# Kernel optimization log

Hardware: AMD Instinct MI355X
Metric: run time of the kernel (lower is better)

## Reference

```python
import jax, jax.numpy as jnp
import numpy as np

KD, KY, KX = 3, 3, 3  # kernel_size from init_kwargs


def setup_inputs() -> dict:
    key = jax.random.key(0)
    x = jax.random.normal(key, (4, 2, 64, 256, 256), dtype=jnp.float32)
    return {"x": x}


def reference(x):
    # x: [B, CH, D, H, W]
    B, CH, D, H, W = x.shape
    pd, py, px = (KD - 1) // 2, (KY - 1) // 2, (KX - 1) // 2
    # replicate padding (torch F.pad mode='replicate' == jnp.pad mode='edge')
    xp = jnp.pad(x, ((0, 0), (0, 0), (pd, pd), (py, py), (px, px)), mode='edge')
    center = (KD * KY * KX) // 2  # flattened center position, excluded from max
    # running max over the 26 non-center neighbors; never materializes the
    # [B, CH, 27, D, H, W] tensor the torch conv3d path creates.
    max_nc = jnp.full(x.shape, -jnp.inf, dtype=x.dtype)
    idx = 0
    for i in range(KD):
        for j in range(KY):
            for k in range(KX):
                if idx != center:
                    shifted = xp[:, :, i:i + D, j:j + H, k:k + W]
                    max_nc = jnp.maximum(max_nc, shifted)
                idx += 1
    mask = x > max_nc  # strict local maximum (excluding self)
    return x * mask.astype(x.dtype)
```

## Files before the change

kernel.cpp:

```cpp
#include <hip/hip_runtime.h>


constexpr int D_   = 64;
constexpr int H_   = 256;
constexpr int W_   = 256;
constexpr int HW_  = H_ * W_;
constexpr int NVOL = 8;
constexpr int DC   = 8;
constexpr int ROWS = 8;
constexpr int SROWS = ROWS + 2;

__device__ __forceinline__ float f3(float a, float b, float c) {
    return fmaxf(fmaxf(a, b), c);
}

__global__ __launch_bounds__(512, 4)
void nms3d(const float* __restrict__ x, float* __restrict__ out)
{
    __shared__ float buf[2][SROWS][W_];

    const int tx = threadIdx.x;
    const int ty = threadIdx.y;
    const int h0 = blockIdx.y * ROWS;
    const int h  = h0 + ty;
    const int n  = blockIdx.z;
    const int z0 = blockIdx.x * DC;
    const int c  = tx << 2;

    const float* __restrict__ base  = x   + (size_t)n * D_ * HW_;
    float* __restrict__       obase = out + (size_t)n * D_ * HW_;

    const int extra = (ty == 0) ? 0 : (ty == ROWS - 1 ? SROWS - 1 : -1);
    const int gx = (extra == 0) ? max(h0 - 1, 0) : min(h0 + ROWS, H_ - 1);

    {
        const float* sp = base + (size_t)max(z0 - 1, 0) * HW_;
        const float4 r = *(const float4*)(sp + h * W_ + c);
        *(float4*)&buf[0][ty + 1][c] = r;
        if (extra >= 0) {
            const float4 rx = *(const float4*)(sp + gx * W_ + c);
            *(float4*)&buf[0][extra][c] = rx;
        }
    }
    __syncthreads();

    float4 vm9_pp = {0,0,0,0};
    float4 vm9_p  = {0,0,0,0};
    float4 cr8_p  = {0,0,0,0};
    float4 vprev  = {0,0,0,0};

#pragma unroll
    for (int t = 0; t < DC + 2; ++t) {
        const int zi  = z0 - 1 + t;
        const int cur = t & 1, nxt = cur ^ 1;

        float4 r, rx;
        const bool do_stage = (t < DC + 1);
        if (do_stage) {
            const float* sp = base + (size_t)min(zi + 1, D_ - 1) * HW_;
            r = *(const float4*)(sp + h * W_ + c);
            if (extra >= 0) rx = *(const float4*)(sp + gx * W_ + c);
        }

        const float4 a = *(const float4*)&buf[cur][ty    ][c];
        const float4 b = *(const float4*)&buf[cur][ty + 1][c];
        const float4 d = *(const float4*)&buf[cur][ty + 2][c];

        float4 va;
        va.x = fmaxf(a.x, d.x); va.y = fmaxf(a.y, d.y);
        va.z = fmaxf(a.z, d.z); va.w = fmaxf(a.w, d.w);

        float vaL = __shfl_up(va.w, 1);   if (tx == 0)  vaL = va.x;
        float vaR = __shfl_down(va.x, 1); if (tx == 63) vaR = va.w;
        float bL  = __shfl_up(b.w, 1);    if (tx == 0)  bL  = b.x;
        float bR  = __shfl_down(b.x, 1);  if (tx == 63) bR  = b.w;

        float4 hv;
        hv.x = f3(vaL, va.x, va.y);  hv.y = f3(va.x, va.y, va.z);
        hv.z = f3(va.y, va.z, va.w); hv.w = f3(va.z, va.w, vaR);
        float4 nb;
        nb.x = fmaxf(bL, b.y);   nb.y = fmaxf(b.x, b.z);
        nb.z = fmaxf(b.y, b.w);  nb.w = fmaxf(b.z, bR);

        float4 c8, cu;
        c8.x = fmaxf(hv.x, nb.x); c8.y = fmaxf(hv.y, nb.y);
        c8.z = fmaxf(hv.z, nb.z); c8.w = fmaxf(hv.w, nb.w);
        cu.x = fmaxf(c8.x, b.x);  cu.y = fmaxf(c8.y, b.y);
        cu.z = fmaxf(c8.z, b.z);  cu.w = fmaxf(c8.w, b.w);

        if (zi > z0) {
            float4 mx, o;
            mx.x = f3(vm9_pp.x, cr8_p.x, cu.x);
            mx.y = f3(vm9_pp.y, cr8_p.y, cu.y);
            mx.z = f3(vm9_pp.z, cr8_p.z, cu.z);
            mx.w = f3(vm9_pp.w, cr8_p.w, cu.w);
            o.x = vprev.x > mx.x ? vprev.x : 0.0f;
            o.y = vprev.y > mx.y ? vprev.y : 0.0f;
            o.z = vprev.z > mx.z ? vprev.z : 0.0f;
            o.w = vprev.w > mx.w ? vprev.w : 0.0f;
            *(float4*)(obase + (size_t)(zi - 1) * HW_ + (size_t)h * W_ + c) = o;
        }
        vm9_pp = vm9_p; vm9_p = cu; cr8_p = c8; vprev = b;

        if (do_stage) {
            *(float4*)&buf[nxt][ty + 1][c] = r;
            if (extra >= 0) *(float4*)&buf[nxt][extra][c] = rx;
        }
        __syncthreads();
    }
}

extern "C" void kernel_launch(void* const* d_in, const int* in_sizes, int n_in,
                              void* d_out, int out_size, void* d_ws, size_t ws_size,
                              hipStream_t stream)
{
    const float* x = (const float*)d_in[0];
    float* out = (float*)d_out;
    dim3 block(64, ROWS, 1);
    dim3 grid(D_ / DC, H_ / ROWS, NVOL);
    nms3d<<<grid, block, 0, stream>>>(x, out);
}
```

Before: 231.6 us.

## Use per-wave async global-to-LDS DMA with triple buffering and no barriers

Each wave now loads its own three neighbor rows per depth slice directly into LDS with global_load_lds, in a three-slot ring buffer prefetched two slices ahead. It tracks completion with hand-tuned s_waitcnt vmcnt values instead of block-wide __syncthreads. Blocks shrink to four rows. This removes barrier stalls and the register round trip for staging. In exchange each row is loaded three times instead of being shared across neighboring rows, and correctness depends on the vmcnt counts matching the exact number of outstanding loads and stores.

New measurement: 232.3 us. Within noise of the previous version (+0.3%).

```diff
diff --git a/kernel.cpp b/kernel.cpp
--- a/kernel.cpp
+++ b/kernel.cpp
@@ -7,22 +7,26 @@
 constexpr int HW_  = H_ * W_;
 constexpr int NVOL = 8;
 constexpr int DC   = 8;
-constexpr int ROWS = 8;
-constexpr int SROWS = ROWS + 2;
 
 __device__ __forceinline__ float f3(float a, float b, float c) {
     return fmaxf(fmaxf(a, b), c);
 }
 
-__global__ __launch_bounds__(512, 4)
+__device__ __forceinline__ void dma_row(const float* g, float* l) {
+    __builtin_amdgcn_global_load_lds(
+        (const __attribute__((address_space(1))) void*)g,
+        (__attribute__((address_space(3))) void*)l,
+        16, 0, 0);
+}
+
+__global__ __launch_bounds__(256, 4)
 void nms3d(const float* __restrict__ x, float* __restrict__ out)
 {
-    __shared__ float buf[2][SROWS][W_];
+    __shared__ float buf[4][3][3][W_];
 
     const int tx = threadIdx.x;
     const int ty = threadIdx.y;
-    const int h0 = blockIdx.y * ROWS;
-    const int h  = h0 + ty;
+    const int h  = (blockIdx.y << 2) + ty;
     const int n  = blockIdx.z;
     const int z0 = blockIdx.x * DC;
     const int c  = tx << 2;
@@ -30,19 +34,20 @@
     const float* __restrict__ base  = x   + (size_t)n * D_ * HW_;
     float* __restrict__       obase = out + (size_t)n * D_ * HW_;
 
-    const int extra = (ty == 0) ? 0 : (ty == ROWS - 1 ? SROWS - 1 : -1);
-    const int gx = (extra == 0) ? max(h0 - 1, 0) : min(h0 + ROWS, H_ - 1);
+    const int r0 = (h == 0)      ? 0      : h - 1;
+    const int r2 = (h == H_ - 1) ? H_ - 1 : h + 1;
 
-    {
-        const float* sp = base + (size_t)max(z0 - 1, 0) * HW_;
-        const float4 r = *(const float4*)(sp + h * W_ + c);
-        *(float4*)&buf[0][ty + 1][c] = r;
-        if (extra >= 0) {
-            const float4 rx = *(const float4*)(sp + gx * W_ + c);
-            *(float4*)&buf[0][extra][c] = rx;
-        }
-    }
-    __syncthreads();
+    auto stage = [&](int s) {
+        const int zc = min(max(z0 - 1 + s, 0), D_ - 1);
+        const float* sp = base + (size_t)zc * HW_;
+        float* slot = &buf[ty][s % 3][0][0];
+        dma_row(sp + r0 * W_ + c, slot);
+        dma_row(sp + h  * W_ + c, slot + W_);
+        dma_row(sp + r2 * W_ + c, slot + 2 * W_);
+    };
+
+    stage(0);
+    stage(1);
 
     float4 vm9_pp = {0,0,0,0};
     float4 vm9_p  = {0,0,0,0};
@@ -51,20 +56,20 @@
 
 #pragma unroll
     for (int t = 0; t < DC + 2; ++t) {
-        const int zi  = z0 - 1 + t;
-        const int cur = t & 1, nxt = cur ^ 1;
+        const int zi = z0 - 1 + t;
 
-        float4 r, rx;
-        const bool do_stage = (t < DC + 1);
-        if (do_stage) {
-            const float* sp = base + (size_t)min(zi + 1, D_ - 1) * HW_;
-            r = *(const float4*)(sp + h * W_ + c);
-            if (extra >= 0) rx = *(const float4*)(sp + gx * W_ + c);
-        }
+        if (t + 2 <= DC + 1) stage(t + 2);
 
-        const float4 a = *(const float4*)&buf[cur][ty    ][c];
-        const float4 b = *(const float4*)&buf[cur][ty + 1][c];
-        const float4 d = *(const float4*)&buf[cur][ty + 2][c];
+        if      (t <= 2) asm volatile("s_waitcnt vmcnt(6)" ::: "memory");
+        else if (t == 3) asm volatile("s_waitcnt vmcnt(7)" ::: "memory");
+        else if (t <= 7) asm volatile("s_waitcnt vmcnt(8)" ::: "memory");
+        else if (t == 8) asm volatile("s_waitcnt vmcnt(5)" ::: "memory");
+        else             asm volatile("s_waitcnt vmcnt(2)" ::: "memory");
+
+        const int sl = t % 3;
+        const float4 a = *(const float4*)&buf[ty][sl][0][c];
+        const float4 b = *(const float4*)&buf[ty][sl][1][c];
+        const float4 d = *(const float4*)&buf[ty][sl][2][c];
 
         float4 va;
         va.x = fmaxf(a.x, d.x); va.y = fmaxf(a.y, d.y);
@@ -101,12 +106,6 @@
             *(float4*)(obase + (size_t)(zi - 1) * HW_ + (size_t)h * W_ + c) = o;
         }
         vm9_pp = vm9_p; vm9_p = cu; cr8_p = c8; vprev = b;
-
-        if (do_stage) {
-            *(float4*)&buf[nxt][ty + 1][c] = r;
-            if (extra >= 0) *(float4*)&buf[nxt][extra][c] = rx;
-        }
-        __syncthreads();
     }
 }
 
@@ -116,7 +115,7 @@
 {
     const float* x = (const float*)d_in[0];
     float* out = (float*)d_out;
-    dim3 block(64, ROWS, 1);
-    dim3 grid(D_ / DC, H_ / ROWS, NVOL);
+    dim3 block(64, 4, 1);
+    dim3 grid(D_ / DC, H_ / 4, NVOL);
     nms3d<<<grid, block, 0, stream>>>(x, out);
 }
```
